# Optimization experiments

Hardware: AMD Instinct MI355X
Metric: run time of the kernel (lower is better)

Reference implementation:

```python
import jax, jax.numpy as jnp
import numpy as np

B, S, D, H = 4, 2048, 256, 4
DH = D // H  # per-head dim (shared for q, k, v)


def setup_inputs() -> dict:
    key = jax.random.key(0)
    ks = jax.random.split(key, 10)
    scale = 1.0 / np.sqrt(D)
    return {
        "q": jax.random.normal(ks[0], (B, S, D), jnp.float32),
        "k": jax.random.normal(ks[1], (B, S, D), jnp.float32),
        "v": jax.random.normal(ks[2], (B, S, D), jnp.float32),
        "mask": jax.random.randint(ks[3], (B, S, S), 0, 2).astype(bool),
        # per-head query/key projections: [H, D, DH] (+ bias [H, DH])
        "Wq": jax.random.uniform(ks[4], (H, D, DH), jnp.float32, -scale, scale),
        "bq": jax.random.uniform(ks[5], (H, DH), jnp.float32, -scale, scale),
        "Wk": jax.random.uniform(ks[6], (H, D, DH), jnp.float32, -scale, scale),
        "bk": jax.random.uniform(ks[7], (H, DH), jnp.float32, -scale, scale),
        # shared value projection: [D, DH]
        "Wv": jax.random.uniform(ks[8], (D, DH), jnp.float32, -scale, scale),
        "bv": jnp.zeros((DH,), jnp.float32),
        # final projection (no bias): [DH, D]
        "Wf": jax.random.uniform(ks[9], (DH, D), jnp.float32, -scale, scale),
    }


def reference(q, k, v, mask, Wq, bq, Wk, bk, Wv, bv, Wf):
    # per-head projections (all heads at once): [B, H, S, DH]
    q_h = jnp.einsum("bsd,hde->bhse", q, Wq) + bq[None, :, None, :]
    k_h = jnp.einsum("bsd,hde->bhse", k, Wk) + bk[None, :, None, :]
    # shared value projection: [B, S, DH]
    v_p = v @ Wv + bv
    # scaled scores: [B, H, S, S]
    scores = jnp.einsum("bhse,bhte->bhst", q_h, k_h) / jnp.sqrt(
        jnp.asarray(DH, q_h.dtype)
    )
    scores = jnp.where(mask[:, None, :, :], jnp.asarray(-1e9, scores.dtype), scores)
    attn = jax.nn.softmax(scores, axis=-1)  # [B, H, S, S]
    # shared V for every head: [B, H, S, DH]
    heads = jnp.einsum("bhst,bte->bhse", attn, v_p)
    mean_head = heads.mean(axis=1)  # [B, S, DH]
    out = mean_head @ Wf  # [B, S, D]
    return out, attn
```

## Files before the change

kernel.cpp:

```cpp
#include <hip/hip_runtime.h>
#include <stdint.h>
#include <stddef.h>

#define B_ 4
#define S_ 2048
#define D_ 256
#define H_ 4
#define DH_ 64
#define NT 128
#define SC_LOG2E 0.18033688011112042f

typedef __attribute__((ext_vector_type(8))) short short8;
typedef __attribute__((ext_vector_type(4))) short short4v;
typedef __attribute__((ext_vector_type(4))) float f32x4;
typedef unsigned int uint;

__device__ __forceinline__ short bf16_rne(float f) {
  union { float f; uint32_t u; } c; c.f = f;
  uint32_t u = c.u + 0x7FFFu + ((c.u >> 16) & 1u);
  return (short)(u >> 16);
}

__device__ __forceinline__ f32x4 mfma16(short8 a, short8 b, f32x4 c) {
  return __builtin_amdgcn_mfma_f32_16x16x32_bf16(a, b, c, 0, 0, 0);
}

__device__ __forceinline__ void gl_lds16(const short* g, short* l) {
  __builtin_amdgcn_global_load_lds(
      (const __attribute__((address_space(1))) unsigned int*)g,
      (__attribute__((address_space(3))) unsigned int*)l, 16, 0, 0);
}

__global__ void prep_weights(const float* __restrict__ Wq, const float* __restrict__ Wk,
                             const float* __restrict__ Wv,
                             short* __restrict__ WqT, short* __restrict__ WkT,
                             short* __restrict__ WvT) {
  int tid = blockIdx.x * blockDim.x + threadIdx.x;
  if (tid < 65536) {
    int n = tid >> 8, d = tid & 255;
    int hh = n >> 6, e = n & 63;
    WqT[tid] = bf16_rne(Wq[((size_t)hh * D_ + d) * DH_ + e]);
    WkT[tid] = bf16_rne(Wk[((size_t)hh * D_ + d) * DH_ + e]);
  } else if (tid < 65536 + 16384) {
    int t2 = tid - 65536;
    int e = t2 >> 8, d = t2 & 255;
    WvT[t2] = bf16_rne(Wv[(size_t)d * DH_ + e]);
  }
}

__global__ void detect_kernel(const unsigned int* __restrict__ m, int* __restrict__ flag) {
  __shared__ int isbool;
  if (threadIdx.x == 0) isbool = 0;
  __syncthreads();
#pragma unroll
  for (int i = 0; i < 4; ++i) {
    unsigned int d = m[threadIdx.x + i * 256];
    if (d & 0xFFFFFFFEu) isbool = 1;
  }
  __syncthreads();
  if (threadIdx.x == 0) *flag = isbool ? 0 : 1;
}

__global__ __launch_bounds__(256) void pack_mask(const unsigned char* __restrict__ maskB,
                                                 const int* __restrict__ flagp,
                                                 uint* __restrict__ mbits) {
  int tid = blockIdx.x * 256 + threadIdx.x;
  uint w = 0;
  if (*flagp) {
    const uint4* p = (const uint4*)((const uint*)maskB + (size_t)tid * 32);
#pragma unroll
    for (int i = 0; i < 8; ++i) {
      uint4 d = p[i];
      w |= (d.x ? 1u : 0u) << (i * 4);
      w |= (d.y ? 1u : 0u) << (i * 4 + 1);
      w |= (d.z ? 1u : 0u) << (i * 4 + 2);
      w |= (d.w ? 1u : 0u) << (i * 4 + 3);
    }
  } else {
    const uint4* p = (const uint4*)(maskB + (size_t)tid * 32);
#pragma unroll
    for (int i = 0; i < 2; ++i) {
      uint4 d = p[i];
      const uint* dw = (const uint*)&d;
#pragma unroll
      for (int j = 0; j < 4; ++j) {
        uint x = dw[j];
        int base = i * 16 + j * 4;
        w |= ((x & 0x000000FFu) ? 1u : 0u) << (base);
        w |= ((x & 0x0000FF00u) ? 1u : 0u) << (base + 1);
        w |= ((x & 0x00FF0000u) ? 1u : 0u) << (base + 2);
        w |= ((x & 0xFF000000u) ? 1u : 0u) << (base + 3);
      }
    }
  }
  mbits[tid] = w;
}

__global__ __launch_bounds__(256) void proj_kernel(
    const float* __restrict__ X, const short* __restrict__ WT,
    const float* __restrict__ bias, short* __restrict__ outp, int vmode) {
  const int b = blockIdx.z;
  const int s0 = blockIdx.x * 64;
  const int n0 = blockIdx.y * 64;
  const int tid = threadIdx.x;
  const int wave = tid >> 6, lane = tid & 63;
  const int lr = lane & 15, lg = lane >> 4;

  const int arowi = s0 + wave * 16 + lr;
  const float* xr = X + ((size_t)b * S_ + arowi) * D_;

  f32x4 zero4 = {0.f, 0.f, 0.f, 0.f};
  f32x4 acc[4];
#pragma unroll
  for (int ct = 0; ct < 4; ++ct) acc[ct] = zero4;

#pragma unroll
  for (int c = 0; c < 8; ++c) {
    const int k0 = c * 32 + lg * 8;
    f32x4 x0 = *(const f32x4*)(xr + k0);
    f32x4 x1 = *(const f32x4*)(xr + k0 + 4);
    short8 a;
#pragma unroll
    for (int jj = 0; jj < 4; ++jj) { a[jj] = bf16_rne(x0[jj]); a[4 + jj] = bf16_rne(x1[jj]); }
#pragma unroll
    for (int ct = 0; ct < 4; ++ct) {
      short8 bw = *(const short8*)(WT + (size_t)(n0 + ct * 16 + lr) * D_ + k0);
      acc[ct] = mfma16(a, bw, acc[ct]);
    }
  }

  if (vmode == 0) {
#pragma unroll
    for (int ct = 0; ct < 4; ++ct) {
      int n = n0 + ct * 16 + lr;
      float bb = bias[n];
      int hh = n >> 6, e = n & 63;
#pragma unroll
      for (int r = 0; r < 4; ++r) {
        int srow = s0 + wave * 16 + lg * 4 + r;
        outp[(((size_t)b * H_ + hh) * S_ + srow) * DH_ + e] = bf16_rne(acc[ct][r] + bb);
      }
    }
  } else {
#pragma unroll
    for (int ct = 0; ct < 4; ++ct) {
      int n = n0 + ct * 16 + lr;
      float bb = bias[n];
      int s4 = s0 + wave * 16 + lg * 4;
      short4v pk;
#pragma unroll
      for (int r = 0; r < 4; ++r) pk[r] = bf16_rne(acc[ct][r] + bb);
      *(short4v*)(outp + ((size_t)b * DH_ + n) * S_ + s4) = pk;
    }
  }
}

__device__ __forceinline__ void stageK(const short* Ksrc, short* dst, int wave, int lane) {
#pragma unroll
  for (int i = 0; i < 4; ++i) {
    int db = i * 256 + wave * 64;
    int d = db + lane;
    int s = (d & ~7) | ((d ^ (d >> 3)) & 7);
    gl_lds16(Ksrc + (size_t)s * 8, dst + (size_t)db * 8);
  }
}

__device__ __forceinline__ void stageV(const short* Vb, int t0, short* dst, int wave, int lane) {
#pragma unroll
  for (int i = 0; i < 4; ++i) {
    int db = i * 256 + wave * 64;
    int d = db + lane;
    int s = (d & ~15) | ((d ^ (d >> 4)) & 15);
    int er = s >> 4, c16 = s & 15;
    gl_lds16(Vb + (size_t)er * S_ + t0 + c16 * 8, dst + (size_t)db * 8);
  }
}

__global__ __launch_bounds__(256) void attn_kernel(
    const short* __restrict__ qh, const short* __restrict__ kh,
    const short* __restrict__ vT, const uint* __restrict__ mbits,
    float* __restrict__ attn, float* __restrict__ heads) {
  __shared__ __align__(16) short Kt[2][NT][DH_];
  __shared__ __align__(16) short Vt[2][DH_][NT];
  __shared__ __align__(16) short Pt[4][16][NT];

  const int b = blockIdx.z, h = blockIdx.y;
  const int q0 = blockIdx.x * 64;
  const int tid = threadIdx.x;
  const int wave = tid >> 6, lane = tid & 63;
  const int lr = lane & 15, lg = lane >> 4;

  const size_t bh = (size_t)b * H_ + h;
  const short* Qb = qh + bh * S_ * DH_;
  const short* Kb = kh + bh * S_ * DH_;
  const short* Vb = vT + (size_t)b * DH_ * S_;

  const int qrow = q0 + wave * 16 + lr;
  const uint* mrow = mbits + ((size_t)b * S_ + qrow) * (S_ / 32);
  float* arow = attn + (bh * S_ + qrow) * S_;

  short8 aq0 = *(const short8*)(Qb + (size_t)qrow * DH_ + lg * 8);
  short8 aq1 = *(const short8*)(Qb + (size_t)qrow * DH_ + 32 + lg * 8);

  short* pw = &Pt[wave][0][0];

  float rsum = 0.f;
  stageK(Kb, &Kt[0][0][0], wave, lane);
  __syncthreads();
  int cur = 0;
  for (int t0 = 0; t0 < S_; t0 += NT) {
    if (t0 + NT < S_) stageK(Kb + (size_t)(t0 + NT) * DH_, &Kt[cur ^ 1][0][0], wave, lane);
    const short* kt = &Kt[cur][0][0];
    uint4 mv = *(const uint4*)(mrow + (t0 >> 5));
#pragma unroll
    for (int j = 0; j < 8; ++j) {
      int row = j * 16 + lr;
      int rs = row & 7;
      short8 bk0 = *(const short8*)(kt + row * 64 + ((lg ^ rs) * 8));
      short8 bk1 = *(const short8*)(kt + row * 64 + (((lg + 4) ^ rs) * 8));
      f32x4 acc = {0.f, 0.f, 0.f, 0.f};
      acc = mfma16(bk0, aq0, acc);
      acc = mfma16(bk1, aq1, acc);
      uint mw = ((const uint*)&mv)[j >> 1];
#pragma unroll
      for (int r = 0; r < 4; ++r) {
        int sh = (j & 1) * 16 + lg * 4 + r;
        float p = ((mw >> sh) & 1u) ? 0.f : __builtin_exp2f(acc[r] * SC_LOG2E);
        rsum += p;
      }
    }
    __syncthreads();
    cur ^= 1;
  }
  rsum += __shfl_xor(rsum, 16);
  rsum += __shfl_xor(rsum, 32);
  const float rinv = 1.0f / rsum;

  f32x4 o[4];
#pragma unroll
  for (int ct = 0; ct < 4; ++ct) o[ct] = (f32x4){0.f, 0.f, 0.f, 0.f};

  stageK(Kb, &Kt[0][0][0], wave, lane);
  stageV(Vb, 0, &Vt[0][0][0], wave, lane);
  __syncthreads();
  cur = 0;
  for (int t0 = 0; t0 < S_; t0 += NT) {
    if (t0 + NT < S_) {
      stageK(Kb + (size_t)(t0 + NT) * DH_, &Kt[cur ^ 1][0][0], wave, lane);
      stageV(Vb, t0 + NT, &Vt[cur ^ 1][0][0], wave, lane);
    }
    const short* kt = &Kt[cur][0][0];
    const short* vt = &Vt[cur][0][0];
    uint4 mv = *(const uint4*)(mrow + (t0 >> 5));
#pragma unroll
    for (int j = 0; j < 8; ++j) {
      int row = j * 16 + lr;
      int rs = row & 7;
      short8 bk0 = *(const short8*)(kt + row * 64 + ((lg ^ rs) * 8));
      short8 bk1 = *(const short8*)(kt + row * 64 + (((lg + 4) ^ rs) * 8));
      f32x4 acc = {0.f, 0.f, 0.f, 0.f};
      acc = mfma16(bk0, aq0, acc);
      acc = mfma16(bk1, aq1, acc);
      uint mw = ((const uint*)&mv)[j >> 1];
      f32x4 pst;
      short4v pk;
#pragma unroll
      for (int r = 0; r < 4; ++r) {
        int sh = (j & 1) * 16 + lg * 4 + r;
        float p = ((mw >> sh) & 1u) ? 0.f : __builtin_exp2f(acc[r] * SC_LOG2E) * rinv;
        pst[r] = p;
        pk[r] = bf16_rne(p);
      }
      *(f32x4*)(arow + t0 + j * 16 + lg * 4) = pst;
      int slot = j * 2 + (lg >> 1);
      *(short4v*)(pw + lr * 128 + ((slot ^ lr) * 8) + (lg & 1) * 4) = pk;
    }
#pragma unroll
    for (int ct = 0; ct < 4; ++ct) {
#pragma unroll
      for (int kc = 0; kc < 4; ++kc) {
        short8 apf = *(const short8*)(pw + lr * 128 + (((kc * 4 + lg) ^ lr) * 8));
        int er = ct * 16 + lr;
        short8 bvf = *(const short8*)(vt + er * 128 + (((kc * 4 + lg) ^ (er & 15)) * 8));
        o[ct] = mfma16(bvf, apf, o[ct]);
      }
    }
    __syncthreads();
    cur ^= 1;
  }

#pragma unroll
  for (int ct = 0; ct < 4; ++ct)
    *(f32x4*)(heads + (bh * S_ + qrow) * DH_ + ct * 16 + lg * 4) = o[ct];
}

__global__ __launch_bounds__(256) void final_kernel(
    const float* __restrict__ heads, const float* __restrict__ Wf,
    float* __restrict__ outp) {
  __shared__ float mean[16][DH_];
  const int row0 = blockIdx.x * 16;
  const int tid = threadIdx.x;
#pragma unroll
  for (int i = 0; i < 4; ++i) {
    int idx = tid + i * 256;
    int r = idx >> 6, e = idx & 63;
    int gs = row0 + r;
    int bb = gs >> 11, ss = gs & (S_ - 1);
    float acc = 0.f;
#pragma unroll
    for (int hh = 0; hh < H_; ++hh)
      acc += heads[(((size_t)bb * H_ + hh) * S_ + ss) * DH_ + e];
    mean[r][e] = acc * 0.25f;
  }
  __syncthreads();
  float acc[16];
#pragma unroll
  for (int r = 0; r < 16; ++r) acc[r] = 0.f;
  for (int e = 0; e < DH_; ++e) {
    float wf = Wf[(size_t)e * D_ + tid];
#pragma unroll
    for (int r = 0; r < 16; ++r) acc[r] += mean[r][e] * wf;
  }
#pragma unroll
  for (int r = 0; r < 16; ++r)
    outp[(size_t)(row0 + r) * D_ + tid] = acc[r];
}

extern "C" void kernel_launch(void* const* d_in, const int* in_sizes, int n_in,
                              void* d_out, int out_size, void* d_ws, size_t ws_size,
                              hipStream_t stream) {
  (void)in_sizes; (void)n_in; (void)out_size; (void)ws_size;
  const float* q  = (const float*)d_in[0];
  const float* k  = (const float*)d_in[1];
  const float* v  = (const float*)d_in[2];
  const unsigned char* mask = (const unsigned char*)d_in[3];
  const float* Wq = (const float*)d_in[4];
  const float* bq = (const float*)d_in[5];
  const float* Wk = (const float*)d_in[6];
  const float* bk = (const float*)d_in[7];
  const float* Wv = (const float*)d_in[8];
  const float* bv = (const float*)d_in[9];
  const float* Wf = (const float*)d_in[10];

  float* out  = (float*)d_out;
  float* attn = out + (size_t)B_ * S_ * D_;

  char* ws = (char*)d_ws;
  short* qh    = (short*)(ws);
  short* kh    = (short*)(ws + 4194304);
  short* vT    = (short*)(ws + 8388608);
  short* WqT   = (short*)(ws + 9437184);
  short* WkT   = (short*)(ws + 9568256);
  short* WvT   = (short*)(ws + 9699328);
  float* heads = (float*)(ws + 9732096);
  int*   flag  = (int*)(ws + 18120704);
  uint*  mbits = (uint*)(ws + 18120768);

  detect_kernel<<<1, 256, 0, stream>>>((const unsigned int*)mask, flag);
  pack_mask<<<2048, 256, 0, stream>>>(mask, flag, mbits);
  prep_weights<<<320, 256, 0, stream>>>(Wq, Wk, Wv, WqT, WkT, WvT);
  proj_kernel<<<dim3(32, 4, B_), 256, 0, stream>>>(q, WqT, bq, qh, 0);
  proj_kernel<<<dim3(32, 4, B_), 256, 0, stream>>>(k, WkT, bk, kh, 0);
  proj_kernel<<<dim3(32, 1, B_), 256, 0, stream>>>(v, WvT, bv, vT, 1);
  attn_kernel<<<dim3(32, H_, B_), 256, 0, stream>>>(qh, kh, vT, mbits, attn, heads);
  final_kernel<<<512, 256, 0, stream>>>(heads, Wf, out);
}
```

Measured before the change: 186.4 us.

## Drop LDS staging of K/V and use single-wave blocks reading directly from global

The attention kernel moves from 256-thread blocks that cooperatively double-buffer K and V tiles into LDS to 64-thread single-wave blocks. Each wave now loads K and V MFMA fragments straight from global memory, leaving only the P tile in LDS. This removes the LDS staging and the block-wide barriers and raises the block count four-fold. In exchange, K/V reuse across the four waves that shared a tile is lost, so global/L2 traffic rises and the loads become less coalesced.

```diff
diff --git a/kernel.cpp b/kernel.cpp
--- a/kernel.cpp
+++ b/kernel.cpp
@@ -23,12 +23,6 @@
 
 __device__ __forceinline__ f32x4 mfma16(short8 a, short8 b, f32x4 c) {
   return __builtin_amdgcn_mfma_f32_16x16x32_bf16(a, b, c, 0, 0, 0);
-}
-
-__device__ __forceinline__ void gl_lds16(const short* g, short* l) {
-  __builtin_amdgcn_global_load_lds(
-      (const __attribute__((address_space(1))) unsigned int*)g,
-      (__attribute__((address_space(3))) unsigned int*)l, 16, 0, 0);
 }
 
 __global__ void prep_weights(const float* __restrict__ Wq, const float* __restrict__ Wk,
@@ -155,39 +149,15 @@
   }
 }
 
-__device__ __forceinline__ void stageK(const short* Ksrc, short* dst, int wave, int lane) {
-#pragma unroll
-  for (int i = 0; i < 4; ++i) {
-    int db = i * 256 + wave * 64;
-    int d = db + lane;
-    int s = (d & ~7) | ((d ^ (d >> 3)) & 7);
-    gl_lds16(Ksrc + (size_t)s * 8, dst + (size_t)db * 8);
-  }
-}
-
-__device__ __forceinline__ void stageV(const short* Vb, int t0, short* dst, int wave, int lane) {
-#pragma unroll
-  for (int i = 0; i < 4; ++i) {
-    int db = i * 256 + wave * 64;
-    int d = db + lane;
-    int s = (d & ~15) | ((d ^ (d >> 4)) & 15);
-    int er = s >> 4, c16 = s & 15;
-    gl_lds16(Vb + (size_t)er * S_ + t0 + c16 * 8, dst + (size_t)db * 8);
-  }
-}
-
-__global__ __launch_bounds__(256) void attn_kernel(
+__global__ __launch_bounds__(64) void attn_kernel(
     const short* __restrict__ qh, const short* __restrict__ kh,
     const short* __restrict__ vT, const uint* __restrict__ mbits,
     float* __restrict__ attn, float* __restrict__ heads) {
-  __shared__ __align__(16) short Kt[2][NT][DH_];
-  __shared__ __align__(16) short Vt[2][DH_][NT];
-  __shared__ __align__(16) short Pt[4][16][NT];
+  __shared__ __align__(16) short Pt[16][NT];
 
   const int b = blockIdx.z, h = blockIdx.y;
-  const int q0 = blockIdx.x * 64;
-  const int tid = threadIdx.x;
-  const int wave = tid >> 6, lane = tid & 63;
+  const int q0 = blockIdx.x * 16;
+  const int lane = threadIdx.x;
   const int lr = lane & 15, lg = lane >> 4;
 
   const size_t bh = (size_t)b * H_ + h;
@@ -195,29 +165,23 @@
   const short* Kb = kh + bh * S_ * DH_;
   const short* Vb = vT + (size_t)b * DH_ * S_;
 
-  const int qrow = q0 + wave * 16 + lr;
+  const int qrow = q0 + lr;
   const uint* mrow = mbits + ((size_t)b * S_ + qrow) * (S_ / 32);
   float* arow = attn + (bh * S_ + qrow) * S_;
 
-  short8 aq0 = *(const short8*)(Qb + (size_t)qrow * DH_ + lg * 8);
-  short8 aq1 = *(const short8*)(Qb + (size_t)qrow * DH_ + 32 + lg * 8);
-
-  short* pw = &Pt[wave][0][0];
+  const short8 aq0 = *(const short8*)(Qb + (size_t)qrow * DH_ + lg * 8);
+  const short8 aq1 = *(const short8*)(Qb + (size_t)qrow * DH_ + 32 + lg * 8);
+
+  short* pw = &Pt[0][0];
 
   float rsum = 0.f;
-  stageK(Kb, &Kt[0][0][0], wave, lane);
-  __syncthreads();
-  int cur = 0;
   for (int t0 = 0; t0 < S_; t0 += NT) {
-    if (t0 + NT < S_) stageK(Kb + (size_t)(t0 + NT) * DH_, &Kt[cur ^ 1][0][0], wave, lane);
-    const short* kt = &Kt[cur][0][0];
     uint4 mv = *(const uint4*)(mrow + (t0 >> 5));
 #pragma unroll
     for (int j = 0; j < 8; ++j) {
-      int row = j * 16 + lr;
-      int rs = row & 7;
-      short8 bk0 = *(const short8*)(kt + row * 64 + ((lg ^ rs) * 8));
-      short8 bk1 = *(const short8*)(kt + row * 64 + (((lg + 4) ^ rs) * 8));
+      const short* kr = Kb + (size_t)(t0 + j * 16 + lr) * DH_ + lg * 8;
+      short8 bk0 = *(const short8*)(kr);
+      short8 bk1 = *(const short8*)(kr + 32);
       f32x4 acc = {0.f, 0.f, 0.f, 0.f};
       acc = mfma16(bk0, aq0, acc);
       acc = mfma16(bk1, aq1, acc);
@@ -229,8 +193,6 @@
         rsum += p;
       }
     }
-    __syncthreads();
-    cur ^= 1;
   }
   rsum += __shfl_xor(rsum, 16);
   rsum += __shfl_xor(rsum, 32);
@@ -240,24 +202,13 @@
 #pragma unroll
   for (int ct = 0; ct < 4; ++ct) o[ct] = (f32x4){0.f, 0.f, 0.f, 0.f};
 
-  stageK(Kb, &Kt[0][0][0], wave, lane);
-  stageV(Vb, 0, &Vt[0][0][0], wave, lane);
-  __syncthreads();
-  cur = 0;
   for (int t0 = 0; t0 < S_; t0 += NT) {
-    if (t0 + NT < S_) {
-      stageK(Kb + (size_t)(t0 + NT) * DH_, &Kt[cur ^ 1][0][0], wave, lane);
-      stageV(Vb, t0 + NT, &Vt[cur ^ 1][0][0], wave, lane);
-    }
-    const short* kt = &Kt[cur][0][0];
-    const short* vt = &Vt[cur][0][0];
     uint4 mv = *(const uint4*)(mrow + (t0 >> 5));
 #pragma unroll
     for (int j = 0; j < 8; ++j) {
-      int row = j * 16 + lr;
-      int rs = row & 7;
-      short8 bk0 = *(const short8*)(kt + row * 64 + ((lg ^ rs) * 8));
-      short8 bk1 = *(const short8*)(kt + row * 64 + (((lg + 4) ^ rs) * 8));
+      const short* kr = Kb + (size_t)(t0 + j * 16 + lr) * DH_ + lg * 8;
+      short8 bk0 = *(const short8*)(kr);
+      short8 bk1 = *(const short8*)(kr + 32);
       f32x4 acc = {0.f, 0.f, 0.f, 0.f};
       acc = mfma16(bk0, aq0, acc);
       acc = mfma16(bk1, aq1, acc);
@@ -280,13 +231,10 @@
 #pragma unroll
       for (int kc = 0; kc < 4; ++kc) {
         short8 apf = *(const short8*)(pw + lr * 128 + (((kc * 4 + lg) ^ lr) * 8));
-        int er = ct * 16 + lr;
-        short8 bvf = *(const short8*)(vt + er * 128 + (((kc * 4 + lg) ^ (er & 15)) * 8));
+        short8 bvf = *(const short8*)(Vb + (size_t)(ct * 16 + lr) * S_ + t0 + kc * 32 + lg * 8);
         o[ct] = mfma16(bvf, apf, o[ct]);
       }
     }
-    __syncthreads();
-    cur ^= 1;
   }
 
 #pragma unroll
@@ -362,6 +310,6 @@
   proj_kernel<<<dim3(32, 4, B_), 256, 0, stream>>>(q, WqT, bq, qh, 0);
   proj_kernel<<<dim3(32, 4, B_), 256, 0, stream>>>(k, WkT, bk, kh, 0);
   proj_kernel<<<dim3(32, 1, B_), 256, 0, stream>>>(v, WvT, bv, vT, 1);
-  attn_kernel<<<dim3(32, H_, B_), 256, 0, stream>>>(qh, kh, vT, mbits, attn, heads);
+  attn_kernel<<<dim3(128, H_, B_), 64, 0, stream>>>(qh, kh, vT, mbits, attn, heads);
   final_kernel<<<512, 256, 0, stream>>>(heads, Wf, out);
 }
```

After: 288.2 us. 1.55x slower.
